# Kernel tuning notes

Hardware: AMD Instinct MI355X
Metric: run time of the kernel (lower is better)

Reference implementation:

```python
import jax, jax.numpy as jnp
import numpy as np

N = 20000
E = 320000
IN_DIM = 128
HIDDEN = 256
HEADS = 4
HD = HIDDEN // HEADS  # 64 per-head channels in layer 1
OUT_DIM = 128
NEG_SLOPE = 0.2
BN_EPS = 1e-5


def setup_inputs() -> dict:
    key = jax.random.key(0)
    ks = jax.random.split(key, 16)
    inp = {
        "x": jax.random.normal(ks[0], (N, IN_DIM), dtype=jnp.float32),
        "edge_index": jax.random.randint(ks[1], (2, E), 0, N, dtype=jnp.int64),
        # layer 1: GATConv(IN_DIM, HD, heads=HEADS, concat=True)
        "W1": jax.random.normal(ks[2], (IN_DIM, HEADS * HD), dtype=jnp.float32) * (1.0 / np.sqrt(IN_DIM)),
        "att_src1": jax.random.normal(ks[3], (HEADS, HD), dtype=jnp.float32) * 0.1,
        "att_dst1": jax.random.normal(ks[4], (HEADS, HD), dtype=jnp.float32) * 0.1,
        "bias1": jnp.zeros((HEADS * HD,), dtype=jnp.float32),
        "bn1_gamma": jnp.ones((HIDDEN,), dtype=jnp.float32),
        "bn1_beta": jnp.zeros((HIDDEN,), dtype=jnp.float32),
        # layer 2: GATConv(HIDDEN, OUT_DIM, heads=1, concat=False)
        "W2": jax.random.normal(ks[5], (HIDDEN, OUT_DIM), dtype=jnp.float32) * (1.0 / np.sqrt(HIDDEN)),
        "att_src2": jax.random.normal(ks[6], (1, OUT_DIM), dtype=jnp.float32) * 0.1,
        "att_dst2": jax.random.normal(ks[7], (1, OUT_DIM), dtype=jnp.float32) * 0.1,
        "bias2": jnp.zeros((OUT_DIM,), dtype=jnp.float32),
        "bn2_gamma": jnp.ones((OUT_DIM,), dtype=jnp.float32),
        "bn2_beta": jnp.zeros((OUT_DIM,), dtype=jnp.float32),
    }
    return inp


def _gat_conv(x, src, dst, W, a_src, a_dst, bias, heads, concat):
    """PyG GATConv with add_self_loops=True (self-loops already in src/dst)."""
    n = x.shape[0]
    hd = W.shape[1] // heads
    h = (x @ W).reshape(n, heads, hd)                     # [N, H, hd]
    alpha_s = jnp.einsum('nhd,hd->nh', h, a_src)          # [N, H]
    alpha_d = jnp.einsum('nhd,hd->nh', h, a_dst)          # [N, H]
    e = alpha_s[src] + alpha_d[dst]                       # [Etot, H]
    e = jnp.where(e > 0, e, NEG_SLOPE * e)                # leaky_relu
    # edge-softmax over incoming edges of each destination node
    m = jax.ops.segment_max(e, dst, num_segments=n)       # [N, H]
    ex = jnp.exp(e - m[dst])
    denom = jax.ops.segment_sum(ex, dst, num_segments=n)  # [N, H]
    alpha = ex / (denom[dst] + 1e-16)                     # [Etot, H]
    msg = h[src] * alpha[..., None]                       # [Etot, H, hd]
    out = jax.ops.segment_sum(msg, dst, num_segments=n)   # [N, H, hd]
    if concat:
        out = out.reshape(n, heads * hd)
    else:
        out = out.mean(axis=1)
    return out + bias


def _batch_norm(x, gamma, beta):
    mean = x.mean(axis=0)
    var = ((x - mean) ** 2).mean(axis=0)  # biased, training-mode BN
    return (x - mean) * jax.lax.rsqrt(var + BN_EPS) * gamma + beta


def reference(x, edge_index, W1, att_src1, att_dst1, bias1, bn1_gamma, bn1_beta,
              W2, att_src2, att_dst2, bias2, bn2_gamma, bn2_beta):
    n = x.shape[0]
    loop = jnp.arange(n, dtype=edge_index.dtype)
    src = jnp.concatenate([edge_index[0], loop])  # add self-loops (PyG default)
    dst = jnp.concatenate([edge_index[1], loop])

    h = _gat_conv(x, src, dst, W1, att_src1, att_dst1, bias1, HEADS, True)
    h = _batch_norm(h, bn1_gamma, bn1_beta)
    h = jax.nn.elu(h)

    h = _gat_conv(h, src, dst, W2, att_src2, att_dst2, bias2, 1, False)
    h = _batch_norm(h, bn2_gamma, bn2_beta)
    return h
```

## Files before the change

kernel.cpp:

```cpp
#include <hip/hip_runtime.h>
#include <type_traits>

constexpr int N_N  = 20000;
constexpr int N_E  = 320000;
constexpr int N_ET = N_E + N_N;
constexpr int IN_D = 128;
constexpr int HID  = 256;
constexpr int H1   = 4;
constexpr int OUTD = 128;
constexpr float SLOPE = 0.2f;
constexpr float BNEPS = 1e-5f;
constexpr int NPART = 32;

typedef unsigned short u16;
typedef float f32x4 __attribute__((ext_vector_type(4)));
typedef short bf16x8 __attribute__((ext_vector_type(8)));

__device__ __forceinline__ float bf2f(u16 u) { return __uint_as_float((unsigned)u << 16); }
__device__ __forceinline__ u16 f2bf(float f) {
  unsigned u = __float_as_uint(f);
  unsigned r = u + 0x7FFFu + ((u >> 16) & 1u);
  return (u16)(r >> 16);
}

__global__ __launch_bounds__(256) void prep_k(const int* __restrict__ ei,
                                              const float* __restrict__ W1,
                                              const float* __restrict__ W2,
                                              u16* __restrict__ wp1,
                                              u16* __restrict__ wp2,
                                              int* __restrict__ cnt) {
  const int i = blockIdx.x * 256 + threadIdx.x;
  if (i < IN_D * HID) {
    const int n = i >> 7, k = i & 127;
    wp1[i] = f2bf(W1[(size_t)k * HID + n]);
  }
  if (i < HID * OUTD) {
    const int n = i >> 8, k = i & 255;
    wp2[i] = f2bf(W2[(size_t)k * OUTD + n]);
  }
  if (i < N_ET) {
    const int dst = (i < N_E) ? ei[N_E + i] : (i - N_E);
    atomicAdd(&cnt[dst], 1);
  }
}

__global__ __launch_bounds__(1024) void scan_k(const int* __restrict__ cnt,
                                               int* __restrict__ rowptr,
                                               int* __restrict__ wcur) {
  __shared__ int wsum[17];
  const int tid = threadIdx.x, lane = tid & 63, wv = tid >> 6;
  constexpr int CHK = 20;
  const int base = tid * CHK;
  int c[CHK];
  int s = 0;
#pragma unroll
  for (int j = 0; j < CHK; ++j) {
    const int idx = base + j;
    c[j] = (idx < N_N) ? cnt[idx] : 0;
    s += c[j];
  }
  const int own = s;
#pragma unroll
  for (int off = 1; off < 64; off <<= 1) {
    const int v = __shfl_up(s, off, 64);
    if (lane >= off) s += v;
  }
  if (lane == 63) wsum[wv] = s;
  __syncthreads();
  if (tid == 0) {
    int run = 0;
#pragma unroll
    for (int i = 0; i < 16; ++i) { const int t = wsum[i]; wsum[i] = run; run += t; }
    wsum[16] = run;
  }
  __syncthreads();
  int run = wsum[wv] + (s - own);
#pragma unroll
  for (int j = 0; j < CHK; ++j) {
    const int idx = base + j;
    if (idx < N_N) {
      rowptr[idx] = run;
      wcur[idx]   = run;
      run += c[j];
    }
  }
  if (tid == 0) rowptr[N_N] = wsum[16];
}

constexpr int GB1 = N_N / 16;
__global__ __launch_bounds__(256) void sg_k(const float* __restrict__ x,
                                            const u16* __restrict__ wp,
                                            const float* __restrict__ asrc,
                                            const float* __restrict__ adst,
                                            u16* __restrict__ h,
                                            float* __restrict__ as_,
                                            float* __restrict__ ad_,
                                            const int* __restrict__ ei,
                                            int* __restrict__ wcur,
                                            int* __restrict__ col) {
  const int tid = threadIdx.x;
  if (blockIdx.x >= GB1) {
    const int i = (blockIdx.x - GB1) * 256 + tid;
    if (i >= N_ET) return;
    int s, dst;
    if (i < N_E) { s = ei[i]; dst = ei[N_E + i]; } else { s = dst = i - N_E; }
    const int pos = atomicAdd(&wcur[dst], 1);
    col[pos] = s;
    return;
  }
  const int wv = tid >> 6, lane = tid & 63;
  const int q = lane >> 4, t = lane & 15;
  const int m0 = blockIdx.x * 16;
  const int n0 = wv * 64;
  f32x4 acc[4] = {};
#pragma unroll
  for (int kb = 0; kb < 4; ++kb) {
    const int k0 = kb * 32 + q * 8;
    const float4 x0 = *(const float4*)(x + (size_t)(m0 + t) * 128 + k0);
    const float4 x1 = *(const float4*)(x + (size_t)(m0 + t) * 128 + k0 + 4);
    bf16x8 a;
    a[0] = (short)f2bf(x0.x); a[1] = (short)f2bf(x0.y);
    a[2] = (short)f2bf(x0.z); a[3] = (short)f2bf(x0.w);
    a[4] = (short)f2bf(x1.x); a[5] = (short)f2bf(x1.y);
    a[6] = (short)f2bf(x1.z); a[7] = (short)f2bf(x1.w);
#pragma unroll
    for (int nt = 0; nt < 4; ++nt) {
      const int n = n0 + nt * 16 + t;
      const bf16x8 b = *(const bf16x8*)(wp + (size_t)n * 128 + k0);
      acc[nt] = __builtin_amdgcn_mfma_f32_16x16x32_bf16(a, b, acc[nt], 0, 0, 0);
    }
  }
  float ps[4] = {0.f, 0.f, 0.f, 0.f}, pd[4] = {0.f, 0.f, 0.f, 0.f};
#pragma unroll
  for (int nt = 0; nt < 4; ++nt) {
    const int coln = n0 + nt * 16 + t;
    const float a_s = asrc[coln], a_d = adst[coln];
#pragma unroll
    for (int r = 0; r < 4; ++r) {
      const float d = acc[nt][r];
      h[(size_t)(m0 + q * 4 + r) * 256 + coln] = f2bf(d);
      ps[r] += d * a_s;
      pd[r] += d * a_d;
    }
  }
#pragma unroll
  for (int off = 1; off < 16; off <<= 1)
#pragma unroll
    for (int r = 0; r < 4; ++r) {
      ps[r] += __shfl_xor(ps[r], off, 64);
      pd[r] += __shfl_xor(pd[r], off, 64);
    }
  if (t == 0) {
#pragma unroll
    for (int r = 0; r < 4; ++r) {
      const int row = m0 + q * 4 + r;
      as_[(size_t)row * 4 + wv] = ps[r];
      ad_[(size_t)row * 4 + wv] = pd[r];
    }
  }
}

__global__ __launch_bounds__(256) void gat_agg1_k(const int* __restrict__ rowptr,
                                                  const int* __restrict__ col,
                                                  const u16* __restrict__ h,
                                                  const float* __restrict__ as_,
                                                  const float* __restrict__ ad_,
                                                  u16* __restrict__ out,
                                                  float* __restrict__ accp) {
  __shared__ int   s_s[4][64];
  __shared__ float s_w[4][64][2];
  __shared__ float st_s[2][256], st_q[2][256];
  const int tid = threadIdx.x;
  const int wv = tid >> 6, lane = tid & 63;
  const int nl = wv >> 1, half = wv & 1;
  const int n = blockIdx.x * 2 + nl;
  const int beg = rowptr[n], end = rowptr[n + 1];
  const int c0 = half * 128 + lane * 2;
  const int hl = lane >> 5;
  const int hb = half * 2;
  const float adv0 = ad_[n * 4 + hb], adv1 = ad_[n * 4 + hb + 1];

  float a0 = 0.f, a1 = 0.f, smh = 0.f;

  for (int j0 = beg; j0 < end; j0 += 64) {
    const int cnt = min(64, end - j0);
    const int j = j0 + lane;
    const int sl = col[(j < end) ? j : beg];
    s_s[wv][lane] = sl;
    const float4 av = *(const float4*)(as_ + (size_t)sl * 4);
    const float* ap = (const float*)&av;
    float e0 = ap[hb] + adv0;     e0 = e0 > 0.f ? e0 : SLOPE * e0;
    float e1 = ap[hb + 1] + adv1; e1 = e1 > 0.f ? e1 : SLOPE * e1;
    s_w[wv][lane][0] = (j < end) ? __expf(e0) : 0.f;
    s_w[wv][lane][1] = (j < end) ? __expf(e1) : 0.f;

    int jj = 0;
    for (; jj + 8 <= cnt; jj += 8) {
      int sv[8]; float wt[8]; ushort2 g[8];
#pragma unroll
      for (int u = 0; u < 8; ++u) {
        sv[u] = s_s[wv][jj + u];
        wt[u] = s_w[wv][jj + u][hl];
      }
#pragma unroll
      for (int u = 0; u < 8; ++u) g[u] = *(const ushort2*)(h + (size_t)sv[u] * 256 + c0);
#pragma unroll
      for (int u = 0; u < 8; ++u) {
        smh += wt[u];
        a0 = fmaf(wt[u], bf2f(g[u].x), a0);
        a1 = fmaf(wt[u], bf2f(g[u].y), a1);
      }
    }
    for (; jj < cnt; ++jj) {
      const int s = s_s[wv][jj];
      const float w = s_w[wv][jj][hl];
      const ushort2 g = *(const ushort2*)(h + (size_t)s * 256 + c0);
      smh += w;
      a0 = fmaf(w, bf2f(g.x), a0);
      a1 = fmaf(w, bf2f(g.y), a1);
    }
  }

  const float r = 1.f / (smh + 1e-16f);
  const float v0 = a0 * r, v1 = a1 * r;
  ushort2 o; o.x = f2bf(v0); o.y = f2bf(v1);
  *(ushort2*)(out + (size_t)n * 256 + c0) = o;

  st_s[nl][c0] = v0;     st_s[nl][c0 + 1] = v1;
  st_q[nl][c0] = v0 * v0; st_q[nl][c0 + 1] = v1 * v1;
  __syncthreads();
  {
    const int c = tid;
    const float s = st_s[0][c] + st_s[1][c];
    const float q = st_q[0][c] + st_q[1][c];
    float* dst = accp + (size_t)(blockIdx.x & (NPART - 1)) * 512;
    atomicAdd(&dst[c], s);
    atomicAdd(&dst[256 + c], q);
  }
}

__global__ __launch_bounds__(256) void gat_agg2_k(const int* __restrict__ rowptr,
                                                  const int* __restrict__ col,
                                                  const u16* __restrict__ h,
                                                  const float* __restrict__ as_,
                                                  const float* __restrict__ ad_,
                                                  u16* __restrict__ out,
                                                  float* __restrict__ accp) {
  __shared__ int   s_s[4][64];
  __shared__ float s_w[4][64];
  __shared__ float st_s[4][128], st_q[4][128];
  const int tid = threadIdx.x;
  const int wv = tid >> 6, lane = tid & 63;
  const int n = blockIdx.x * 4 + wv;
  const int beg = rowptr[n], end = rowptr[n + 1];
  const int c0 = lane * 2;
  const float adv = ad_[n];

  float a0 = 0.f, a1 = 0.f, smh = 0.f;

  for (int j0 = beg; j0 < end; j0 += 64) {
    const int cnt = min(64, end - j0);
    const int j = j0 + lane;
    const int sl = col[(j < end) ? j : beg];
    s_s[wv][lane] = sl;
    float e = as_[sl] + adv;
    e = e > 0.f ? e : SLOPE * e;
    s_w[wv][lane] = (j < end) ? __expf(e) : 0.f;

    int jj = 0;
    for (; jj + 8 <= cnt; jj += 8) {
      int sv[8]; float wt[8]; ushort2 g[8];
#pragma unroll
      for (int u = 0; u < 8; ++u) {
        sv[u] = s_s[wv][jj + u];
        wt[u] = s_w[wv][jj + u];
      }
#pragma unroll
      for (int u = 0; u < 8; ++u) g[u] = *(const ushort2*)(h + (size_t)sv[u] * 128 + c0);
#pragma unroll
      for (int u = 0; u < 8; ++u) {
        smh += wt[u];
        a0 = fmaf(wt[u], bf2f(g[u].x), a0);
        a1 = fmaf(wt[u], bf2f(g[u].y), a1);
      }
    }
    for (; jj < cnt; ++jj) {
      const int s = s_s[wv][jj];
      const float w = s_w[wv][jj];
      const ushort2 g = *(const ushort2*)(h + (size_t)s * 128 + c0);
      smh += w;
      a0 = fmaf(w, bf2f(g.x), a0);
      a1 = fmaf(w, bf2f(g.y), a1);
    }
  }

  const float r = 1.f / (smh + 1e-16f);
  const float v0 = a0 * r, v1 = a1 * r;
  ushort2 o; o.x = f2bf(v0); o.y = f2bf(v1);
  *(ushort2*)(out + (size_t)n * 128 + c0) = o;

  st_s[wv][c0] = v0;      st_s[wv][c0 + 1] = v1;
  st_q[wv][c0] = v0 * v0; st_q[wv][c0 + 1] = v1 * v1;
  __syncthreads();
  if (tid < 128) {
    const int c = tid;
    const float s = st_s[0][c] + st_s[1][c] + st_s[2][c] + st_s[3][c];
    const float q = st_q[0][c] + st_q[1][c] + st_q[2][c] + st_q[3][c];
    float* dst = accp + (size_t)(blockIdx.x & (NPART - 1)) * 256;
    atomicAdd(&dst[c], s);
    atomicAdd(&dst[128 + c], q);
  }
}

__global__ __launch_bounds__(256) void gemm2_mfma_k(const u16* __restrict__ hin,
                                                    const float* __restrict__ accp,
                                                    const float* __restrict__ g1,
                                                    const float* __restrict__ b1,
                                                    const u16* __restrict__ wp,
                                                    const float* __restrict__ asrc,
                                                    const float* __restrict__ adst,
                                                    u16* __restrict__ h2,
                                                    float* __restrict__ as_,
                                                    float* __restrict__ ad_) {
  __shared__ float scsh[512];
  __shared__ float red[2][32][2];
  const int tid = threadIdx.x;
  {
    float s = 0.f, q = 0.f;
#pragma unroll
    for (int p = 0; p < NPART; ++p) {
      s += accp[(size_t)p * 512 + tid];
      q += accp[(size_t)p * 512 + 256 + tid];
    }
    const float mean = s * (1.f / N_N);
    const float var  = q * (1.f / N_N) - mean * mean;
    const float inv  = rsqrtf(var + BNEPS);
    const float sc   = g1[tid] * inv;
    scsh[tid]       = sc;
    scsh[256 + tid] = b1[tid] - mean * sc;
  }
  __syncthreads();
  const int wv = tid >> 6, lane = tid & 63;
  const int q = lane >> 4, t = lane & 15;
  const int mh = wv >> 1, nh = wv & 1;
  const int m0 = blockIdx.x * 32 + mh * 16;
  const int n0 = nh * 64;
  f32x4 acc[4] = {};
#pragma unroll
  for (int kb = 0; kb < 8; ++kb) {
    const int k0 = kb * 32 + q * 8;
    const ushort4 u0 = *(const ushort4*)(hin + (size_t)(m0 + t) * 256 + k0);
    const ushort4 u1 = *(const ushort4*)(hin + (size_t)(m0 + t) * 256 + k0 + 4);
    const float4 sc0 = *(const float4*)(scsh + k0);
    const float4 sc1 = *(const float4*)(scsh + k0 + 4);
    const float4 sh0 = *(const float4*)(scsh + 256 + k0);
    const float4 sh1 = *(const float4*)(scsh + 256 + k0 + 4);
    float v[8];
    v[0] = bf2f(u0.x) * sc0.x + sh0.x;
    v[1] = bf2f(u0.y) * sc0.y + sh0.y;
    v[2] = bf2f(u0.z) * sc0.z + sh0.z;
    v[3] = bf2f(u0.w) * sc0.w + sh0.w;
    v[4] = bf2f(u1.x) * sc1.x + sh1.x;
    v[5] = bf2f(u1.y) * sc1.y + sh1.y;
    v[6] = bf2f(u1.z) * sc1.z + sh1.z;
    v[7] = bf2f(u1.w) * sc1.w + sh1.w;
    bf16x8 a;
#pragma unroll
    for (int j = 0; j < 8; ++j) {
      const float e = v[j] > 0.f ? v[j] : __expf(v[j]) - 1.f;
      a[j] = (short)f2bf(e);
    }
#pragma unroll
    for (int nt = 0; nt < 4; ++nt) {
      const int n = n0 + nt * 16 + t;
      const bf16x8 b = *(const bf16x8*)(wp + (size_t)n * 256 + k0);
      acc[nt] = __builtin_amdgcn_mfma_f32_16x16x32_bf16(a, b, acc[nt], 0, 0, 0);
    }
  }
  float ps[4] = {0.f, 0.f, 0.f, 0.f}, pd[4] = {0.f, 0.f, 0.f, 0.f};
#pragma unroll
  for (int nt = 0; nt < 4; ++nt) {
    const int coln = n0 + nt * 16 + t;
    const float a_s = asrc[coln], a_d = adst[coln];
#pragma unroll
    for (int r = 0; r < 4; ++r) {
      const float d = acc[nt][r];
      h2[(size_t)(m0 + q * 4 + r) * 128 + coln] = f2bf(d);
      ps[r] += d * a_s;
      pd[r] += d * a_d;
    }
  }
#pragma unroll
  for (int off = 1; off < 16; off <<= 1)
#pragma unroll
    for (int r = 0; r < 4; ++r) {
      ps[r] += __shfl_xor(ps[r], off, 64);
      pd[r] += __shfl_xor(pd[r], off, 64);
    }
  if (t == 0) {
#pragma unroll
    for (int r = 0; r < 4; ++r) {
      red[0][mh * 16 + q * 4 + r][nh] = ps[r];
      red[1][mh * 16 + q * 4 + r][nh] = pd[r];
    }
  }
  __syncthreads();
  if (tid < 32) {
    as_[(size_t)blockIdx.x * 32 + tid] = red[0][tid][0] + red[0][tid][1];
    ad_[(size_t)blockIdx.x * 32 + tid] = red[1][tid][0] + red[1][tid][1];
  }
}

__global__ __launch_bounds__(256) void apply_k(const u16* __restrict__ X,
                                               const float* __restrict__ accp,
                                               const float* __restrict__ gamma,
                                               const float* __restrict__ beta,
                                               float* __restrict__ Y) {
  __shared__ float s_sc[128], s_sh[128];
  const int tid = threadIdx.x;
  if (tid < 128) {
    float s = 0.f, q = 0.f;
#pragma unroll
    for (int p = 0; p < NPART; ++p) {
      s += accp[(size_t)p * 256 + tid];
      q += accp[(size_t)p * 256 + 128 + tid];
    }
    const float mean = s * (1.f / N_N);
    const float var  = q * (1.f / N_N) - mean * mean;
    const float inv  = rsqrtf(var + BNEPS);
    const float sc   = gamma[tid] * inv;
    s_sc[tid] = sc;
    s_sh[tid] = beta[tid] - mean * sc;
  }
  __syncthreads();
  constexpr size_t TOT = (size_t)N_N * OUTD;
  for (size_t i = ((size_t)blockIdx.x * 256 + tid) * 4; i < TOT;
       i += (size_t)gridDim.x * 256 * 4) {
    const ushort4 u = *(const ushort4*)(X + i);
    const int c = (int)(i & 127);
    float4 o;
    o.x = bf2f(u.x) * s_sc[c]     + s_sh[c];
    o.y = bf2f(u.y) * s_sc[c + 1] + s_sh[c + 1];
    o.z = bf2f(u.z) * s_sc[c + 2] + s_sh[c + 2];
    o.w = bf2f(u.w) * s_sc[c + 3] + s_sh[c + 3];
    *(float4*)(Y + i) = o;
  }
}

constexpr size_t OFF_WP1  = 0;
constexpr size_t OFF_WP2  = OFF_WP1  + (size_t)IN_D * HID / 2;
constexpr size_t OFF_H1   = OFF_WP2  + (size_t)HID * OUTD / 2;
constexpr size_t OFF_OUT1 = OFF_H1   + (size_t)N_N * HID / 2;
constexpr size_t OFF_H2   = OFF_OUT1 + (size_t)N_N * HID / 2;
constexpr size_t OFF_OUT2 = OFF_H2   + (size_t)N_N * OUTD / 2;
constexpr size_t OFF_AS1  = OFF_OUT2 + (size_t)N_N * OUTD / 2;
constexpr size_t OFF_AD1  = OFF_AS1  + (size_t)N_N * H1;
constexpr size_t OFF_AS2  = OFF_AD1  + (size_t)N_N * H1;
constexpr size_t OFF_AD2  = OFF_AS2  + (size_t)N_N;
constexpr size_t OFF_ROWP = OFF_AD2  + (size_t)N_N;
constexpr size_t OFF_COL  = OFF_ROWP + (size_t)(N_N + 1);
constexpr size_t OFF_WCUR = OFF_COL  + (size_t)N_ET;
constexpr size_t OFF_CNT  = OFF_WCUR + (size_t)N_N;
constexpr size_t OFF_ACC1 = OFF_CNT  + (size_t)N_N;
constexpr size_t OFF_ACC2 = OFF_ACC1 + (size_t)NPART * 512;
constexpr size_t OFF_ZEND = OFF_ACC2 + (size_t)NPART * 256;

extern "C" void kernel_launch(void* const* d_in, const int* in_sizes, int n_in,
                              void* d_out, int out_size, void* d_ws, size_t ws_size,
                              hipStream_t stream) {
  const float* x      = (const float*)d_in[0];
  const int*   ei     = (const int*)d_in[1];
  const float* W1     = (const float*)d_in[2];
  const float* asrc1  = (const float*)d_in[3];
  const float* adst1  = (const float*)d_in[4];
  const float* g1     = (const float*)d_in[6];
  const float* b1     = (const float*)d_in[7];
  const float* W2     = (const float*)d_in[8];
  const float* asrc2  = (const float*)d_in[9];
  const float* adst2  = (const float*)d_in[10];
  const float* g2     = (const float*)d_in[12];
  const float* b2     = (const float*)d_in[13];

  float* ws = (float*)d_ws;
  u16*   wp1   = (u16*)(ws + OFF_WP1);
  u16*   wp2   = (u16*)(ws + OFF_WP2);
  u16*   h1    = (u16*)(ws + OFF_H1);
  u16*   out1  = (u16*)(ws + OFF_OUT1);
  u16*   h2    = (u16*)(ws + OFF_H2);
  u16*   out2  = (u16*)(ws + OFF_OUT2);
  float* as1   = ws + OFF_AS1;
  float* ad1   = ws + OFF_AD1;
  float* as2   = ws + OFF_AS2;
  float* ad2   = ws + OFF_AD2;
  int*   rowp  = (int*)(ws + OFF_ROWP);
  int*   col   = (int*)(ws + OFF_COL);
  int*   wcur  = (int*)(ws + OFF_WCUR);
  int*   cnt   = (int*)(ws + OFF_CNT);
  float* acc1p = ws + OFF_ACC1;
  float* acc2p = ws + OFF_ACC2;
  float* outf  = (float*)d_out;

  hipMemsetAsync(cnt, 0, (OFF_ZEND - OFF_CNT) * sizeof(float), stream);

  const int eb = (N_ET + 255) / 256;
  prep_k<<<eb, 256, 0, stream>>>(ei, W1, W2, wp1, wp2, cnt);
  scan_k<<<1, 1024, 0, stream>>>(cnt, rowp, wcur);
  sg_k<<<GB1 + eb, 256, 0, stream>>>(x, wp1, asrc1, adst1, h1, as1, ad1, ei, wcur, col);
  gat_agg1_k<<<N_N / 2, 256, 0, stream>>>(rowp, col, h1, as1, ad1, out1, acc1p);
  gemm2_mfma_k<<<N_N / 32, 256, 0, stream>>>(out1, acc1p, g1, b1, wp2, asrc2, adst2, h2, as2, ad2);
  gat_agg2_k<<<N_N / 4, 256, 0, stream>>>(rowp, col, h2, as2, ad2, out2, acc2p);
  apply_k<<<512, 256, 0, stream>>>(out2, acc2p, g2, b2, outf);
}
```

Before: 246.3 us.

## Widen aggregation gathers to 16-byte loads and move BN stats to separate kernels

Both GAT aggregation kernels now load 8 bf16 channels per lane with uint4 gathers, splitting the wave across edges (2 or 4 edges in parallel) and combining partial sums with cross-lane shuffles. Layer 1 now handles one node per wave instead of two waves per node. The batch-norm statistics, previously built with per-block shared reductions and partitioned atomics inside the aggregation kernels, move to a dedicated bn_stats kernel that reads back the bf16 outputs. The aim is fewer, wider memory transactions and less epilogue overhead in the gather kernels. The cost is two extra launches, an extra read of each output, and statistics now computed from bf16-rounded values.

```diff
diff --git a/kernel.cpp b/kernel.cpp
--- a/kernel.cpp
+++ b/kernel.cpp
@@ -10,7 +10,6 @@
 constexpr int OUTD = 128;
 constexpr float SLOPE = 0.2f;
 constexpr float BNEPS = 1e-5f;
-constexpr int NPART = 32;
 
 typedef unsigned short u16;
 typedef float f32x4 __attribute__((ext_vector_type(4)));
@@ -21,6 +20,9 @@
   unsigned u = __float_as_uint(f);
   unsigned r = u + 0x7FFFu + ((u >> 16) & 1u);
   return (u16)(r >> 16);
+}
+__device__ __forceinline__ unsigned packbf2(float a, float b) {
+  return (unsigned)f2bf(a) | ((unsigned)f2bf(b) << 16);
 }
 
 __global__ __launch_bounds__(256) void prep_k(const int* __restrict__ ei,
@@ -165,22 +167,21 @@
                                                   const u16* __restrict__ h,
                                                   const float* __restrict__ as_,
                                                   const float* __restrict__ ad_,
-                                                  u16* __restrict__ out,
-                                                  float* __restrict__ accp) {
+                                                  u16* __restrict__ out) {
   __shared__ int   s_s[4][64];
-  __shared__ float s_w[4][64][2];
-  __shared__ float st_s[2][256], st_q[2][256];
+  __shared__ float s_w[4][64][4];
   const int tid = threadIdx.x;
   const int wv = tid >> 6, lane = tid & 63;
-  const int nl = wv >> 1, half = wv & 1;
-  const int n = blockIdx.x * 2 + nl;
+  const int n = blockIdx.x * 4 + wv;
   const int beg = rowptr[n], end = rowptr[n + 1];
-  const int c0 = half * 128 + lane * 2;
-  const int hl = lane >> 5;
-  const int hb = half * 2;
-  const float adv0 = ad_[n * 4 + hb], adv1 = ad_[n * 4 + hb + 1];
-
-  float a0 = 0.f, a1 = 0.f, smh = 0.f;
+  const int half = lane >> 5;
+  const int il = lane & 31;
+  const int head = il >> 3;
+  const float4 advv = *(const float4*)(ad_ + (size_t)n * 4);
+  const float adv[4] = {advv.x, advv.y, advv.z, advv.w};
+
+  float acc[8] = {};
+  float smh = 0.f;
 
   for (int j0 = beg; j0 < end; j0 += 64) {
     const int cnt = min(64, end - j0);
@@ -189,53 +190,68 @@
     s_s[wv][lane] = sl;
     const float4 av = *(const float4*)(as_ + (size_t)sl * 4);
     const float* ap = (const float*)&av;
-    float e0 = ap[hb] + adv0;     e0 = e0 > 0.f ? e0 : SLOPE * e0;
-    float e1 = ap[hb + 1] + adv1; e1 = e1 > 0.f ? e1 : SLOPE * e1;
-    s_w[wv][lane][0] = (j < end) ? __expf(e0) : 0.f;
-    s_w[wv][lane][1] = (j < end) ? __expf(e1) : 0.f;
-
-    int jj = 0;
-    for (; jj + 8 <= cnt; jj += 8) {
-      int sv[8]; float wt[8]; ushort2 g[8];
-#pragma unroll
-      for (int u = 0; u < 8; ++u) {
-        sv[u] = s_s[wv][jj + u];
-        wt[u] = s_w[wv][jj + u][hl];
+#pragma unroll
+    for (int hh = 0; hh < 4; ++hh) {
+      float e = ap[hh] + adv[hh];
+      e = e > 0.f ? e : SLOPE * e;
+      s_w[wv][lane][hh] = (j < end) ? __expf(e) : 0.f;
+    }
+
+    const int npairs = (cnt + 1) >> 1;
+    int p = 0;
+    for (; p + 4 <= npairs; p += 4) {
+      int sv[4]; float wt[4]; uint4 g[4];
+#pragma unroll
+      for (int u = 0; u < 4; ++u) {
+        const int e = 2 * (p + u) + half;
+        sv[u] = s_s[wv][e];
+        wt[u] = s_w[wv][e][head];
       }
 #pragma unroll
-      for (int u = 0; u < 8; ++u) g[u] = *(const ushort2*)(h + (size_t)sv[u] * 256 + c0);
-#pragma unroll
-      for (int u = 0; u < 8; ++u) {
+      for (int u = 0; u < 4; ++u)
+        g[u] = *(const uint4*)(h + (size_t)sv[u] * 256 + il * 8);
+#pragma unroll
+      for (int u = 0; u < 4; ++u) {
         smh += wt[u];
-        a0 = fmaf(wt[u], bf2f(g[u].x), a0);
-        a1 = fmaf(wt[u], bf2f(g[u].y), a1);
+        const unsigned* gd = (const unsigned*)&g[u];
+#pragma unroll
+        for (int d = 0; d < 4; ++d) {
+          const float lo = __uint_as_float(gd[d] << 16);
+          const float hi = __uint_as_float(gd[d] & 0xFFFF0000u);
+          acc[2 * d]     = fmaf(wt[u], lo, acc[2 * d]);
+          acc[2 * d + 1] = fmaf(wt[u], hi, acc[2 * d + 1]);
+        }
       }
     }
-    for (; jj < cnt; ++jj) {
-      const int s = s_s[wv][jj];
-      const float w = s_w[wv][jj][hl];
-      const ushort2 g = *(const ushort2*)(h + (size_t)s * 256 + c0);
+    for (; p < npairs; ++p) {
+      const int e = 2 * p + half;
+      const int s = s_s[wv][e];
+      const float w = s_w[wv][e][head];
+      const uint4 g = *(const uint4*)(h + (size_t)s * 256 + il * 8);
       smh += w;
-      a0 = fmaf(w, bf2f(g.x), a0);
-      a1 = fmaf(w, bf2f(g.y), a1);
-    }
-  }
-
-  const float r = 1.f / (smh + 1e-16f);
-  const float v0 = a0 * r, v1 = a1 * r;
-  ushort2 o; o.x = f2bf(v0); o.y = f2bf(v1);
-  *(ushort2*)(out + (size_t)n * 256 + c0) = o;
-
-  st_s[nl][c0] = v0;     st_s[nl][c0 + 1] = v1;
-  st_q[nl][c0] = v0 * v0; st_q[nl][c0 + 1] = v1 * v1;
-  __syncthreads();
-  {
-    const int c = tid;
-    const float s = st_s[0][c] + st_s[1][c];
-    const float q = st_q[0][c] + st_q[1][c];
-    float* dst = accp + (size_t)(blockIdx.x & (NPART - 1)) * 512;
-    atomicAdd(&dst[c], s);
-    atomicAdd(&dst[256 + c], q);
+      const unsigned* gd = (const unsigned*)&g;
+#pragma unroll
+      for (int d = 0; d < 4; ++d) {
+        const float lo = __uint_as_float(gd[d] << 16);
+        const float hi = __uint_as_float(gd[d] & 0xFFFF0000u);
+        acc[2 * d]     = fmaf(w, lo, acc[2 * d]);
+        acc[2 * d + 1] = fmaf(w, hi, acc[2 * d + 1]);
+      }
+    }
+  }
+
+#pragma unroll
+  for (int k = 0; k < 8; ++k) acc[k] += __shfl_xor(acc[k], 32, 64);
+  smh += __shfl_xor(smh, 32, 64);
+
+  if (half == 0) {
+    const float r = 1.f / (smh + 1e-16f);
+    uint4 o;
+    unsigned* op = (unsigned*)&o;
+#pragma unroll
+    for (int d = 0; d < 4; ++d)
+      op[d] = packbf2(acc[2 * d] * r, acc[2 * d + 1] * r);
+    *(uint4*)(out + (size_t)n * 256 + il * 8) = o;
   }
 }
 
@@ -244,19 +260,19 @@
                                                   const u16* __restrict__ h,
                                                   const float* __restrict__ as_,
                                                   const float* __restrict__ ad_,
-                                                  u16* __restrict__ out,
-                                                  float* __restrict__ accp) {
+                                                  u16* __restrict__ out) {
   __shared__ int   s_s[4][64];
   __shared__ float s_w[4][64];
-  __shared__ float st_s[4][128], st_q[4][128];
   const int tid = threadIdx.x;
   const int wv = tid >> 6, lane = tid & 63;
   const int n = blockIdx.x * 4 + wv;
   const int beg = rowptr[n], end = rowptr[n + 1];
-  const int c0 = lane * 2;
+  const int grp = lane >> 4;
+  const int il = lane & 15;
   const float adv = ad_[n];
 
-  float a0 = 0.f, a1 = 0.f, smh = 0.f;
+  float acc[8] = {};
+  float smh = 0.f;
 
   for (int j0 = beg; j0 < end; j0 += 64) {
     const int cnt = min(64, end - j0);
@@ -267,53 +283,83 @@
     e = e > 0.f ? e : SLOPE * e;
     s_w[wv][lane] = (j < end) ? __expf(e) : 0.f;
 
-    int jj = 0;
-    for (; jj + 8 <= cnt; jj += 8) {
-      int sv[8]; float wt[8]; ushort2 g[8];
-#pragma unroll
-      for (int u = 0; u < 8; ++u) {
-        sv[u] = s_s[wv][jj + u];
-        wt[u] = s_w[wv][jj + u];
+    const int nq = (cnt + 3) >> 2;
+    int p = 0;
+    for (; p + 4 <= nq; p += 4) {
+      int sv[4]; float wt[4]; uint4 g[4];
+#pragma unroll
+      for (int u = 0; u < 4; ++u) {
+        const int e4 = 4 * (p + u) + grp;
+        sv[u] = s_s[wv][e4];
+        wt[u] = s_w[wv][e4];
       }
 #pragma unroll
-      for (int u = 0; u < 8; ++u) g[u] = *(const ushort2*)(h + (size_t)sv[u] * 128 + c0);
-#pragma unroll
-      for (int u = 0; u < 8; ++u) {
+      for (int u = 0; u < 4; ++u)
+        g[u] = *(const uint4*)(h + (size_t)sv[u] * 128 + il * 8);
+#pragma unroll
+      for (int u = 0; u < 4; ++u) {
         smh += wt[u];
-        a0 = fmaf(wt[u], bf2f(g[u].x), a0);
-        a1 = fmaf(wt[u], bf2f(g[u].y), a1);
+        const unsigned* gd = (const unsigned*)&g[u];
+#pragma unroll
+        for (int d = 0; d < 4; ++d) {
+          const float lo = __uint_as_float(gd[d] << 16);
+          const float hi = __uint_as_float(gd[d] & 0xFFFF0000u);
+          acc[2 * d]     = fmaf(wt[u], lo, acc[2 * d]);
+          acc[2 * d + 1] = fmaf(wt[u], hi, acc[2 * d + 1]);
+        }
       }
     }
-    for (; jj < cnt; ++jj) {
-      const int s = s_s[wv][jj];
-      const float w = s_w[wv][jj];
-      const ushort2 g = *(const ushort2*)(h + (size_t)s * 128 + c0);
+    for (; p < nq; ++p) {
+      const int e4 = 4 * p + grp;
+      const int s = s_s[wv][e4];
+      const float w = s_w[wv][e4];
+      const uint4 g = *(const uint4*)(h + (size_t)s * 128 + il * 8);
       smh += w;
-      a0 = fmaf(w, bf2f(g.x), a0);
-      a1 = fmaf(w, bf2f(g.y), a1);
-    }
-  }
-
-  const float r = 1.f / (smh + 1e-16f);
-  const float v0 = a0 * r, v1 = a1 * r;
-  ushort2 o; o.x = f2bf(v0); o.y = f2bf(v1);
-  *(ushort2*)(out + (size_t)n * 128 + c0) = o;
-
-  st_s[wv][c0] = v0;      st_s[wv][c0 + 1] = v1;
-  st_q[wv][c0] = v0 * v0; st_q[wv][c0 + 1] = v1 * v1;
-  __syncthreads();
-  if (tid < 128) {
-    const int c = tid;
-    const float s = st_s[0][c] + st_s[1][c] + st_s[2][c] + st_s[3][c];
-    const float q = st_q[0][c] + st_q[1][c] + st_q[2][c] + st_q[3][c];
-    float* dst = accp + (size_t)(blockIdx.x & (NPART - 1)) * 256;
-    atomicAdd(&dst[c], s);
-    atomicAdd(&dst[128 + c], q);
-  }
+      const unsigned* gd = (const unsigned*)&g;
+#pragma unroll
+      for (int d = 0; d < 4; ++d) {
+        const float lo = __uint_as_float(gd[d] << 16);
+        const float hi = __uint_as_float(gd[d] & 0xFFFF0000u);
+        acc[2 * d]     = fmaf(w, lo, acc[2 * d]);
+        acc[2 * d + 1] = fmaf(w, hi, acc[2 * d + 1]);
+      }
+    }
+  }
+
+#pragma unroll
+  for (int k = 0; k < 8; ++k) {
+    acc[k] += __shfl_xor(acc[k], 16, 64);
+    acc[k] += __shfl_xor(acc[k], 32, 64);
+  }
+  smh += __shfl_xor(smh, 16, 64);
+  smh += __shfl_xor(smh, 32, 64);
+
+  if (grp == 0) {
+    const float r = 1.f / (smh + 1e-16f);
+    uint4 o;
+    unsigned* op = (unsigned*)&o;
+#pragma unroll
+    for (int d = 0; d < 4; ++d)
+      op[d] = packbf2(acc[2 * d] * r, acc[2 * d + 1] * r);
+    *(uint4*)(out + (size_t)n * 128 + il * 8) = o;
+  }
+}
+
+template<int CH>
+__global__ __launch_bounds__(CH) void bn_stats_k(const u16* __restrict__ X,
+                                                 float* __restrict__ acc, int n) {
+  const int c = threadIdx.x;
+  float s = 0.f, ss = 0.f;
+  for (int r = blockIdx.x; r < n; r += gridDim.x) {
+    const float v = bf2f(X[(size_t)r * CH + c]);
+    s += v; ss += v * v;
+  }
+  atomicAdd(&acc[c], s);
+  atomicAdd(&acc[CH + c], ss);
 }
 
 __global__ __launch_bounds__(256) void gemm2_mfma_k(const u16* __restrict__ hin,
-                                                    const float* __restrict__ accp,
+                                                    const float* __restrict__ acc1,
                                                     const float* __restrict__ g1,
                                                     const float* __restrict__ b1,
                                                     const u16* __restrict__ wp,
@@ -326,14 +372,8 @@
   __shared__ float red[2][32][2];
   const int tid = threadIdx.x;
   {
-    float s = 0.f, q = 0.f;
-#pragma unroll
-    for (int p = 0; p < NPART; ++p) {
-      s += accp[(size_t)p * 512 + tid];
-      q += accp[(size_t)p * 512 + 256 + tid];
-    }
-    const float mean = s * (1.f / N_N);
-    const float var  = q * (1.f / N_N) - mean * mean;
+    const float mean = acc1[tid] * (1.f / N_N);
+    const float var  = acc1[256 + tid] * (1.f / N_N) - mean * mean;
     const float inv  = rsqrtf(var + BNEPS);
     const float sc   = g1[tid] * inv;
     scsh[tid]       = sc;
@@ -412,21 +452,15 @@
 }
 
 __global__ __launch_bounds__(256) void apply_k(const u16* __restrict__ X,
-                                               const float* __restrict__ accp,
+                                               const float* __restrict__ acc,
                                                const float* __restrict__ gamma,
                                                const float* __restrict__ beta,
                                                float* __restrict__ Y) {
   __shared__ float s_sc[128], s_sh[128];
   const int tid = threadIdx.x;
   if (tid < 128) {
-    float s = 0.f, q = 0.f;
-#pragma unroll
-    for (int p = 0; p < NPART; ++p) {
-      s += accp[(size_t)p * 256 + tid];
-      q += accp[(size_t)p * 256 + 128 + tid];
-    }
-    const float mean = s * (1.f / N_N);
-    const float var  = q * (1.f / N_N) - mean * mean;
+    const float mean = acc[tid] * (1.f / N_N);
+    const float var  = acc[128 + tid] * (1.f / N_N) - mean * mean;
     const float inv  = rsqrtf(var + BNEPS);
     const float sc   = gamma[tid] * inv;
     s_sc[tid] = sc;
@@ -462,8 +496,8 @@
 constexpr size_t OFF_WCUR = OFF_COL  + (size_t)N_ET;
 constexpr size_t OFF_CNT  = OFF_WCUR + (size_t)N_N;
 constexpr size_t OFF_ACC1 = OFF_CNT  + (size_t)N_N;
-constexpr size_t OFF_ACC2 = OFF_ACC1 + (size_t)NPART * 512;
-constexpr size_t OFF_ZEND = OFF_ACC2 + (size_t)NPART * 256;
+constexpr size_t OFF_ACC2 = OFF_ACC1 + 512;
+constexpr size_t OFF_ZEND = OFF_ACC2 + 256;
 
 extern "C" void kernel_launch(void* const* d_in, const int* in_sizes, int n_in,
                               void* d_out, int out_size, void* d_ws, size_t ws_size,
@@ -496,8 +530,8 @@
   int*   col   = (int*)(ws + OFF_COL);
   int*   wcur  = (int*)(ws + OFF_WCUR);
   int*   cnt   = (int*)(ws + OFF_CNT);
-  float* acc1p = ws + OFF_ACC1;
-  float* acc2p = ws + OFF_ACC2;
+  float* acc1  = ws + OFF_ACC1;
+  float* acc2  = ws + OFF_ACC2;
   float* outf  = (float*)d_out;
 
   hipMemsetAsync(cnt, 0, (OFF_ZEND - OFF_CNT) * sizeof(float), stream);
@@ -506,8 +540,10 @@
   prep_k<<<eb, 256, 0, stream>>>(ei, W1, W2, wp1, wp2, cnt);
   scan_k<<<1, 1024, 0, stream>>>(cnt, rowp, wcur);
   sg_k<<<GB1 + eb, 256, 0, stream>>>(x, wp1, asrc1, adst1, h1, as1, ad1, ei, wcur, col);
-  gat_agg1_k<<<N_N / 2, 256, 0, stream>>>(rowp, col, h1, as1, ad1, out1, acc1p);
-  gemm2_mfma_k<<<N_N / 32, 256, 0, stream>>>(out1, acc1p, g1, b1, wp2, asrc2, adst2, h2, as2, ad2);
-  gat_agg2_k<<<N_N / 4, 256, 0, stream>>>(rowp, col, h2, as2, ad2, out2, acc2p);
-  apply_k<<<512, 256, 0, stream>>>(out2, acc2p, g2, b2, outf);
-}
+  gat_agg1_k<<<N_N / 4, 256, 0, stream>>>(rowp, col, h1, as1, ad1, out1);
+  bn_stats_k<HID><<<512, HID, 0, stream>>>(out1, acc1, N_N);
+  gemm2_mfma_k<<<N_N / 32, 256, 0, stream>>>(out1, acc1, g1, b1, wp2, asrc2, adst2, h2, as2, ad2);
+  gat_agg2_k<<<N_N / 4, 256, 0, stream>>>(rowp, col, h2, as2, ad2, out2);
+  bn_stats_k<OUTD><<<512, OUTD, 0, stream>>>(out2, acc2, N_N);
+  apply_k<<<512, 256, 0, stream>>>(out2, acc2, g2, b2, outf);
+}
```

Result: slower. 274.3 us (+11.3%).

## Move BatchNorm statistics out of aggregation kernels into separate reduction kernels

Applied to the files above, without the earlier changes.

Removes the per-block shared-memory staging, __syncthreads and partitioned atomics for BatchNorm sums from both GAT aggregation kernels. Adds a standalone bn_stats kernel that rereads the bf16 aggregated output column-wise and atomically accumulates sums and squares into a single buffer. This takes the barrier and the atomic contention off the latency-bound gather kernels, at the cost of two extra launches and an extra pass over the output. Statistics now come from bf16-rounded values rather than fp32.

```diff
diff --git a/kernel.cpp b/kernel.cpp
--- a/kernel.cpp
+++ b/kernel.cpp
@@ -10,7 +10,6 @@
 constexpr int OUTD = 128;
 constexpr float SLOPE = 0.2f;
 constexpr float BNEPS = 1e-5f;
-constexpr int NPART = 32;
 
 typedef unsigned short u16;
 typedef float f32x4 __attribute__((ext_vector_type(4)));
@@ -165,11 +164,9 @@
                                                   const u16* __restrict__ h,
                                                   const float* __restrict__ as_,
                                                   const float* __restrict__ ad_,
-                                                  u16* __restrict__ out,
-                                                  float* __restrict__ accp) {
+                                                  u16* __restrict__ out) {
   __shared__ int   s_s[4][64];
   __shared__ float s_w[4][64][2];
-  __shared__ float st_s[2][256], st_q[2][256];
   const int tid = threadIdx.x;
   const int wv = tid >> 6, lane = tid & 63;
   const int nl = wv >> 1, half = wv & 1;
@@ -222,21 +219,8 @@
   }
 
   const float r = 1.f / (smh + 1e-16f);
-  const float v0 = a0 * r, v1 = a1 * r;
-  ushort2 o; o.x = f2bf(v0); o.y = f2bf(v1);
+  ushort2 o; o.x = f2bf(a0 * r); o.y = f2bf(a1 * r);
   *(ushort2*)(out + (size_t)n * 256 + c0) = o;
-
-  st_s[nl][c0] = v0;     st_s[nl][c0 + 1] = v1;
-  st_q[nl][c0] = v0 * v0; st_q[nl][c0 + 1] = v1 * v1;
-  __syncthreads();
-  {
-    const int c = tid;
-    const float s = st_s[0][c] + st_s[1][c];
-    const float q = st_q[0][c] + st_q[1][c];
-    float* dst = accp + (size_t)(blockIdx.x & (NPART - 1)) * 512;
-    atomicAdd(&dst[c], s);
-    atomicAdd(&dst[256 + c], q);
-  }
 }
 
 __global__ __launch_bounds__(256) void gat_agg2_k(const int* __restrict__ rowptr,
@@ -244,11 +228,9 @@
                                                   const u16* __restrict__ h,
                                                   const float* __restrict__ as_,
                                                   const float* __restrict__ ad_,
-                                                  u16* __restrict__ out,
-                                                  float* __restrict__ accp) {
+                                                  u16* __restrict__ out) {
   __shared__ int   s_s[4][64];
   __shared__ float s_w[4][64];
-  __shared__ float st_s[4][128], st_q[4][128];
   const int tid = threadIdx.x;
   const int wv = tid >> 6, lane = tid & 63;
   const int n = blockIdx.x * 4 + wv;
@@ -295,25 +277,25 @@
   }
 
   const float r = 1.f / (smh + 1e-16f);
-  const float v0 = a0 * r, v1 = a1 * r;
-  ushort2 o; o.x = f2bf(v0); o.y = f2bf(v1);
+  ushort2 o; o.x = f2bf(a0 * r); o.y = f2bf(a1 * r);
   *(ushort2*)(out + (size_t)n * 128 + c0) = o;
-
-  st_s[wv][c0] = v0;      st_s[wv][c0 + 1] = v1;
-  st_q[wv][c0] = v0 * v0; st_q[wv][c0 + 1] = v1 * v1;
-  __syncthreads();
-  if (tid < 128) {
-    const int c = tid;
-    const float s = st_s[0][c] + st_s[1][c] + st_s[2][c] + st_s[3][c];
-    const float q = st_q[0][c] + st_q[1][c] + st_q[2][c] + st_q[3][c];
-    float* dst = accp + (size_t)(blockIdx.x & (NPART - 1)) * 256;
-    atomicAdd(&dst[c], s);
-    atomicAdd(&dst[128 + c], q);
-  }
+}
+
+template<int CH>
+__global__ __launch_bounds__(CH) void bn_stats_k(const u16* __restrict__ X,
+                                                 float* __restrict__ acc, int n) {
+  const int c = threadIdx.x;
+  float s = 0.f, ss = 0.f;
+  for (int r = blockIdx.x; r < n; r += gridDim.x) {
+    const float v = bf2f(X[(size_t)r * CH + c]);
+    s += v; ss += v * v;
+  }
+  atomicAdd(&acc[c], s);
+  atomicAdd(&acc[CH + c], ss);
 }
 
 __global__ __launch_bounds__(256) void gemm2_mfma_k(const u16* __restrict__ hin,
-                                                    const float* __restrict__ accp,
+                                                    const float* __restrict__ acc1,
                                                     const float* __restrict__ g1,
                                                     const float* __restrict__ b1,
                                                     const u16* __restrict__ wp,
@@ -326,14 +308,8 @@
   __shared__ float red[2][32][2];
   const int tid = threadIdx.x;
   {
-    float s = 0.f, q = 0.f;
-#pragma unroll
-    for (int p = 0; p < NPART; ++p) {
-      s += accp[(size_t)p * 512 + tid];
-      q += accp[(size_t)p * 512 + 256 + tid];
-    }
-    const float mean = s * (1.f / N_N);
-    const float var  = q * (1.f / N_N) - mean * mean;
+    const float mean = acc1[tid] * (1.f / N_N);
+    const float var  = acc1[256 + tid] * (1.f / N_N) - mean * mean;
     const float inv  = rsqrtf(var + BNEPS);
     const float sc   = g1[tid] * inv;
     scsh[tid]       = sc;
@@ -412,21 +388,15 @@
 }
 
 __global__ __launch_bounds__(256) void apply_k(const u16* __restrict__ X,
-                                               const float* __restrict__ accp,
+                                               const float* __restrict__ acc,
                                                const float* __restrict__ gamma,
                                                const float* __restrict__ beta,
                                                float* __restrict__ Y) {
   __shared__ float s_sc[128], s_sh[128];
   const int tid = threadIdx.x;
   if (tid < 128) {
-    float s = 0.f, q = 0.f;
-#pragma unroll
-    for (int p = 0; p < NPART; ++p) {
-      s += accp[(size_t)p * 256 + tid];
-      q += accp[(size_t)p * 256 + 128 + tid];
-    }
-    const float mean = s * (1.f / N_N);
-    const float var  = q * (1.f / N_N) - mean * mean;
+    const float mean = acc[tid] * (1.f / N_N);
+    const float var  = acc[128 + tid] * (1.f / N_N) - mean * mean;
     const float inv  = rsqrtf(var + BNEPS);
     const float sc   = gamma[tid] * inv;
     s_sc[tid] = sc;
@@ -462,8 +432,8 @@
 constexpr size_t OFF_WCUR = OFF_COL  + (size_t)N_ET;
 constexpr size_t OFF_CNT  = OFF_WCUR + (size_t)N_N;
 constexpr size_t OFF_ACC1 = OFF_CNT  + (size_t)N_N;
-constexpr size_t OFF_ACC2 = OFF_ACC1 + (size_t)NPART * 512;
-constexpr size_t OFF_ZEND = OFF_ACC2 + (size_t)NPART * 256;
+constexpr size_t OFF_ACC2 = OFF_ACC1 + 512;
+constexpr size_t OFF_ZEND = OFF_ACC2 + 256;
 
 extern "C" void kernel_launch(void* const* d_in, const int* in_sizes, int n_in,
                               void* d_out, int out_size, void* d_ws, size_t ws_size,
@@ -496,8 +466,8 @@
   int*   col   = (int*)(ws + OFF_COL);
   int*   wcur  = (int*)(ws + OFF_WCUR);
   int*   cnt   = (int*)(ws + OFF_CNT);
-  float* acc1p = ws + OFF_ACC1;
-  float* acc2p = ws + OFF_ACC2;
+  float* acc1  = ws + OFF_ACC1;
+  float* acc2  = ws + OFF_ACC2;
   float* outf  = (float*)d_out;
 
   hipMemsetAsync(cnt, 0, (OFF_ZEND - OFF_CNT) * sizeof(float), stream);
@@ -506,8 +476,10 @@
   prep_k<<<eb, 256, 0, stream>>>(ei, W1, W2, wp1, wp2, cnt);
   scan_k<<<1, 1024, 0, stream>>>(cnt, rowp, wcur);
   sg_k<<<GB1 + eb, 256, 0, stream>>>(x, wp1, asrc1, adst1, h1, as1, ad1, ei, wcur, col);
-  gat_agg1_k<<<N_N / 2, 256, 0, stream>>>(rowp, col, h1, as1, ad1, out1, acc1p);
-  gemm2_mfma_k<<<N_N / 32, 256, 0, stream>>>(out1, acc1p, g1, b1, wp2, asrc2, adst2, h2, as2, ad2);
-  gat_agg2_k<<<N_N / 4, 256, 0, stream>>>(rowp, col, h2, as2, ad2, out2, acc2p);
-  apply_k<<<512, 256, 0, stream>>>(out2, acc2p, g2, b2, outf);
-}
+  gat_agg1_k<<<N_N / 2, 256, 0, stream>>>(rowp, col, h1, as1, ad1, out1);
+  bn_stats_k<HID><<<512, HID, 0, stream>>>(out1, acc1, N_N);
+  gemm2_mfma_k<<<N_N / 32, 256, 0, stream>>>(out1, acc1, g1, b1, wp2, asrc2, adst2, h2, as2, ad2);
+  gat_agg2_k<<<N_N / 4, 256, 0, stream>>>(rowp, col, h2, as2, ad2, out2);
+  bn_stats_k<OUTD><<<512, OUTD, 0, stream>>>(out2, acc2, N_N);
+  apply_k<<<512, 256, 0, stream>>>(out2, acc2, g2, b2, outf);
+}
```

Result: slower. 302.0 us (+22.6%).
